# Optimization experiments

Hardware: AMD Instinct MI355X
Metric: run time of the kernel (lower is better)

The kernel has to match this reference:

```python
import jax, jax.numpy as jnp
from jax import lax
import numpy as np

B = 32        # graphs per batch
NN = 513      # nodes per graph (odd M so Y/Z head lengths match)
IN = 128      # input_dim
OUT = 256     # output_dim
T = 4         # edge_types
STEPS = 4     # ggnn propagation steps
DEG = 16
N = B * NN
E = N * DEG
CAT = IN + OUT


def setup_inputs() -> dict:
    key = jax.random.key(0)
    ks = jax.random.split(key, 16)
    f32 = jnp.float32
    feature = jax.random.normal(ks[0], (N, IN), f32)
    offs = (jnp.arange(B) * NN)[:, None]
    edge_src = (jax.random.randint(ks[1], (B, NN * DEG), 0, NN) + offs).reshape(-1)
    edge_dst = (jax.random.randint(ks[2], (B, NN * DEG), 0, NN) + offs).reshape(-1)
    edge_type = jax.random.randint(ks[3], (E,), 0, T)
    s = 1.0 / np.sqrt(OUT)
    W_msg = jax.random.normal(ks[4], (T, OUT, OUT), f32) * s      # [T, out, in] (torch Linear layout)
    b_msg = jnp.zeros((T, OUT), f32)
    gru_w_ih = jax.random.normal(ks[5], (3 * OUT, OUT), f32) * s
    gru_w_hh = jax.random.normal(ks[6], (3 * OUT, OUT), f32) * s
    gru_b_ih = jnp.zeros((3 * OUT,), f32)
    gru_b_hh = jnp.zeros((3 * OUT,), f32)
    conv1_w = jax.random.normal(ks[7], (OUT, OUT, 3), f32) * (1.0 / np.sqrt(OUT * 3))
    conv1_b = jnp.zeros((OUT,), f32)
    conv2_w = jax.random.normal(ks[8], (OUT, OUT, 1), f32) * s
    conv2_b = jnp.zeros((OUT,), f32)
    convc1_w = jax.random.normal(ks[9], (CAT, CAT, 3), f32) * (1.0 / np.sqrt(CAT * 3))
    convc1_b = jnp.zeros((CAT,), f32)
    convc2_w = jax.random.normal(ks[10], (CAT, CAT, 2), f32) * (1.0 / np.sqrt(CAT * 2))
    convc2_b = jnp.zeros((CAT,), f32)
    mlpy_w = jax.random.normal(ks[11], (1, OUT), f32) * s
    mlpy_b = jnp.zeros((1,), f32)
    mlpz_w = jax.random.normal(ks[12], (1, CAT), f32) * (1.0 / np.sqrt(CAT))
    mlpz_b = jnp.zeros((1,), f32)
    return dict(feature=feature, W_msg=W_msg, b_msg=b_msg,
                gru_w_ih=gru_w_ih, gru_w_hh=gru_w_hh, gru_b_ih=gru_b_ih, gru_b_hh=gru_b_hh,
                conv1_w=conv1_w, conv1_b=conv1_b, conv2_w=conv2_w, conv2_b=conv2_b,
                convc1_w=convc1_w, convc1_b=convc1_b, convc2_w=convc2_w, convc2_b=convc2_b,
                mlpy_w=mlpy_w, mlpy_b=mlpy_b, mlpz_w=mlpz_w, mlpz_b=mlpz_b,
                edge_src=edge_src, edge_dst=edge_dst, edge_type=edge_type)


def _conv1d(x, w, b):
    # x: [B, C_in, L], w: [C_out, C_in, K]
    y = lax.conv_general_dilated(x, w, (1,), 'VALID', dimension_numbers=('NCH', 'OIH', 'NCH'))
    return y + b[None, :, None]


def _maxpool1d(x, k, s):
    init = jnp.array(-jnp.inf, dtype=x.dtype)
    return lax.reduce_window(x, init, lax.max, (1, 1, k), (1, 1, s), 'VALID')


def _forward(feature, W_msg, b_msg, gru_w_ih, gru_w_hh, gru_b_ih, gru_b_hh,
             conv1_w, conv1_b, conv2_w, conv2_b, convc1_w, convc1_b, convc2_w, convc2_b,
             mlpy_w, mlpy_b, mlpz_w, mlpz_b, edge_src, edge_dst, edge_type):
    # --- GatedGraphConv (DGL semantics): zero-pad features to out_feats ---
    h = jnp.pad(feature, ((0, 0), (0, OUT - IN)))  # [N, OUT]
    for _ in range(STEPS):
        # per-etype linear on all nodes: hw[t] = h @ W_msg[t].T + b_msg[t]
        hw = jnp.einsum('nd,tod->tno', h, W_msg) + b_msg[:, None, :]   # [T, N, OUT]
        msg = hw[edge_type, edge_src]                                   # [E, OUT] gather
        a = jax.ops.segment_sum(msg, edge_dst, num_segments=N)          # [N, OUT] scatter-add
        # GRUCell(a, h) in torch gate order (r, z, n)
        gi = a @ gru_w_ih.T + gru_b_ih
        gh = h @ gru_w_hh.T + gru_b_hh
        ir, iz, inn = jnp.split(gi, 3, axis=-1)
        hr, hz, hn = jnp.split(gh, 3, axis=-1)
        r = jax.nn.sigmoid(ir + hr)
        z = jax.nn.sigmoid(iz + hz)
        n = jnp.tanh(inn + r * hn)
        h = (1.0 - z) * n + z * h
    outputs = h                                             # [N, OUT]
    ci = jnp.concatenate([outputs, feature], axis=-1)       # [N, OUT+IN]
    # batchify to [B, C, L]
    hi = outputs.reshape(B, NN, OUT).transpose(0, 2, 1)
    cb = ci.reshape(B, NN, CAT).transpose(0, 2, 1)
    Y1 = _maxpool1d(jax.nn.relu(_conv1d(hi, conv1_w, conv1_b)), 3, 2)
    Y2 = _maxpool1d(jax.nn.relu(_conv1d(Y1, conv2_w, conv2_b)), 2, 2).transpose(0, 2, 1)   # [B, 127, OUT]
    Z1 = _maxpool1d(jax.nn.relu(_conv1d(cb, convc1_w, convc1_b)), 3, 2)
    Z2 = _maxpool1d(jax.nn.relu(_conv1d(Z1, convc2_w, convc2_b)), 2, 2).transpose(0, 2, 1)  # [B, 127, CAT]
    before_avg = (Y2 @ mlpy_w.T + mlpy_b) * (Z2 @ mlpz_w.T + mlpz_b)   # [B, 127, 1]
    avg = before_avg.mean(axis=1)                                       # [B, 1]
    return jax.nn.sigmoid(avg).squeeze(-1)                              # [B]


def reference(feature, W_msg, b_msg, gru_w_ih, gru_w_hh, gru_b_ih, gru_b_hh,
              conv1_w, conv1_b, conv2_w, conv2_b, convc1_w, convc1_b, convc2_w, convc2_b,
              mlpy_w, mlpy_b, mlpz_w, mlpz_b, edge_src, edge_dst, edge_type):
    return _forward(feature, W_msg, b_msg, gru_w_ih, gru_w_hh, gru_b_ih, gru_b_hh,
                    conv1_w, conv1_b, conv2_w, conv2_b, convc1_w, convc1_b, convc2_w, convc2_b,
                    mlpy_w, mlpy_b, mlpz_w, mlpz_b, edge_src, edge_dst, edge_type)
```

## Files before the change

### kernel.cpp

```cpp
#include <hip/hip_runtime.h>

#define Bg    32
#define NNg   513
#define INF   128
#define OUTF  256
#define TT    4
#define NSTEP 4
#define DEGg  16
#define Ntot  (Bg*NNg)
#define Etot  (Ntot*DEGg)
#define CATF  (OUTF+INF)
#define SK    1056
#define NSB   65

typedef _Float16 h8_t __attribute__((ext_vector_type(8)));
typedef float    f4_t __attribute__((ext_vector_type(4)));

__global__ void pad_h_k(const float* __restrict__ feat, float* __restrict__ h,
                        _Float16* __restrict__ h16) {
  int idx = blockIdx.x*256 + threadIdx.x;
  if (idx >= Ntot*OUTF) return;
  int n = idx >> 8, c = idx & 255;
  float v = (c < INF) ? feat[n*INF + c] : 0.f;
  h[idx] = v;
  h16[idx] = (_Float16)v;
}

__global__ void cvt_k(const float* __restrict__ s, _Float16* __restrict__ d, int n) {
  int i = (blockIdx.x*256 + threadIdx.x) * 4;
  if (i >= n) return;
  float4 v = *reinterpret_cast<const float4*>(s + i);
  _Float16 o[4] = {(_Float16)v.x, (_Float16)v.y, (_Float16)v.z, (_Float16)v.w};
  *reinterpret_cast<ushort4*>(d + i) = *reinterpret_cast<ushort4*>(o);
}

__global__ void build_cb16_k(const _Float16* __restrict__ h16,
                             const float* __restrict__ feat,
                             _Float16* __restrict__ cb) {
  int idx = blockIdx.x*256 + threadIdx.x;
  if (idx >= Ntot*CATF) return;
  int n = idx / CATF, c = idx % CATF;
  cb[idx] = (c < OUTF) ? h16[n*OUTF + c] : (_Float16)feat[n*INF + (c - OUTF)];
}

__global__ void zero_int_k(int* __restrict__ p, int n) {
  int i = blockIdx.x*256 + threadIdx.x;
  if (i < n) p[i] = 0;
}

__global__ void hist_k(const int* __restrict__ dst, int* __restrict__ cnt) {
  int e = blockIdx.x*256 + threadIdx.x;
  if (e < Etot) atomicAdd(&cnt[dst[e]], 1);
}

__global__ void scan1_k(const int* __restrict__ cnt, int* __restrict__ rowptr,
                        int* __restrict__ bsum) {
  __shared__ int buf[256];
  int t = threadIdx.x;
  int i = blockIdx.x*256 + t;
  int v = (i < Ntot) ? cnt[i] : 0;
  buf[t] = v;
  __syncthreads();
  #pragma unroll
  for (int off = 1; off < 256; off <<= 1) {
    int x = (t >= off) ? buf[t - off] : 0;
    __syncthreads();
    buf[t] += x;
    __syncthreads();
  }
  if (i < Ntot) rowptr[i] = buf[t] - v;
  if (t == 255) bsum[blockIdx.x] = buf[255];
}

__global__ void scan2_k(int* __restrict__ bsum) {
  __shared__ int buf[256];
  int t = threadIdx.x;
  int v = (t < NSB) ? bsum[t] : 0;
  buf[t] = v;
  __syncthreads();
  #pragma unroll
  for (int off = 1; off < 256; off <<= 1) {
    int x = (t >= off) ? buf[t - off] : 0;
    __syncthreads();
    buf[t] += x;
    __syncthreads();
  }
  if (t < NSB) bsum[t] = buf[t] - v;
}

__global__ void scan3_k(int* __restrict__ rowptr, const int* __restrict__ bsum) {
  int i = blockIdx.x*256 + threadIdx.x;
  if (i < Ntot) rowptr[i] += bsum[blockIdx.x];
  if (i == 0) rowptr[Ntot] = Etot;
}

__global__ void fill_k(const int* __restrict__ dst, const int* __restrict__ rowptr,
                       int* __restrict__ cursor, int* __restrict__ eidx) {
  int e = blockIdx.x*256 + threadIdx.x;
  if (e < Etot) {
    int d = dst[e];
    int pos = atomicAdd(&cursor[d], 1);
    eidx[rowptr[d] + pos] = e;
  }
}

__global__ void gather_k(const _Float16* __restrict__ h16, const int* __restrict__ rowptr,
                         const int* __restrict__ eidx, const int* __restrict__ esrc,
                         const int* __restrict__ etyp, _Float16* __restrict__ s16) {
  __shared__ int src_s[128];
  __shared__ int typ_s[128];
  int n = blockIdx.x;
  int c = threadIdx.x;
  int s0 = rowptr[n], e0 = rowptr[n+1];
  float a0 = 0.f, a1 = 0.f, a2 = 0.f, a3 = 0.f;
  int c0 = 0, c1 = 0, c2 = 0, c3 = 0;
  for (int base = s0; base < e0; base += 128) {
    int m = e0 - base; if (m > 128) m = 128;
    if (c < m) {
      int ee = eidx[base + c];
      src_s[c] = esrc[ee];
      typ_s[c] = etyp[ee];
    }
    __syncthreads();
    for (int i = 0; i < m; ++i) {
      int t = typ_s[i];
      float v = (float)h16[(size_t)src_s[i]*256 + c];
      a0 += (t == 0) ? v : 0.f;
      a1 += (t == 1) ? v : 0.f;
      a2 += (t == 2) ? v : 0.f;
      a3 += (t == 3) ? v : 0.f;
      c0 += (t == 0); c1 += (t == 1); c2 += (t == 2); c3 += (t == 3);
    }
    __syncthreads();
  }
  size_t b = (size_t)n * SK;
  s16[b + 0*256 + c] = (_Float16)a0;
  s16[b + 1*256 + c] = (_Float16)a1;
  s16[b + 2*256 + c] = (_Float16)a2;
  s16[b + 3*256 + c] = (_Float16)a3;
  if (c < 32) {
    float cv = (c == 0) ? (float)c0 : (c == 1) ? (float)c1 :
               (c == 2) ? (float)c2 : (c == 3) ? (float)c3 : 0.f;
    s16[b + 1024 + c] = (_Float16)cv;
  }
}

__global__ void repack_wext_k(const float* __restrict__ Wmsg, const float* __restrict__ bmsg,
                              _Float16* __restrict__ wext) {
  int idx = blockIdx.x*256 + threadIdx.x;
  if (idx >= 256*SK) return;
  int co = idx / SK, k = idx % SK;
  float v;
  if (k < 1024)      { int t = k >> 8, ci = k & 255; v = Wmsg[((size_t)t*256 + co)*256 + ci]; }
  else if (k < 1028) { v = bmsg[(k - 1024)*256 + co]; }
  else               { v = 0.f; }
  wext[idx] = (_Float16)v;
}

__global__ void gru_gate_k(const float* __restrict__ gi, const float* __restrict__ gh,
                           float* __restrict__ h, _Float16* __restrict__ h16) {
  int idx = blockIdx.x*256 + threadIdx.x;
  if (idx >= Ntot*OUTF) return;
  int n = idx >> 8, g = idx & 255;
  const float* gin = gi + (size_t)n*768;
  const float* ghn = gh + (size_t)n*768;
  float r  = 1.f / (1.f + expf(-(gin[g]       + ghn[g])));
  float z  = 1.f / (1.f + expf(-(gin[256 + g] + ghn[256 + g])));
  float nn = tanhf(gin[512 + g] + r * ghn[512 + g]);
  float hv = h[idx];
  float o = (1.f - z) * nn + z * hv;
  h[idx] = o;
  h16[idx] = (_Float16)o;
}

template<typename OT>
__global__ void maxpool_k(const float* __restrict__ in, OT* __restrict__ out,
                          int Lin, int Lp, int C, int kwin) {
  int idx = blockIdx.x*256 + threadIdx.x;
  int total = Bg*Lp*C;
  if (idx >= total) return;
  int c = idx % C; int r = idx / C; int p = r % Lp; int b = r / Lp;
  const float* base = in + ((size_t)(b*Lin + 2*p))*C + c;
  float v = base[0];
  for (int w = 1; w < kwin; ++w) v = fmaxf(v, base[(size_t)w*C]);
  out[idx] = (OT)v;
}

__global__ void repack16_k(const float* __restrict__ w, _Float16* __restrict__ wk,
                           int Cout, int Cin, int K) {
  int idx = blockIdx.x*256 + threadIdx.x;
  int total = Cout*Cin*K;
  if (idx >= total) return;
  int ci = idx % Cin; int r = idx / Cin; int k = r % K; int co = r / K;
  wk[idx] = (_Float16)w[(co*Cin + ci)*K + k];
}

__global__ void head_k(const float* __restrict__ Y2, const float* __restrict__ Z2,
                       const float* __restrict__ wy, const float* __restrict__ by,
                       const float* __restrict__ wz, const float* __restrict__ bz,
                       float* __restrict__ out) {
  int b = blockIdx.x;
  int tid = threadIdx.x;
  __shared__ float red[128];
  float sum = 0.f;
  for (int p = tid; p < 127; p += 128) {
    const float* yr = Y2 + ((size_t)(b*127 + p))*OUTF;
    const float* zr = Z2 + ((size_t)(b*127 + p))*CATF;
    float yv = by[0], zv = bz[0];
    for (int c = 0; c < OUTF; ++c) yv = fmaf(yr[c], wy[c], yv);
    for (int c = 0; c < CATF; ++c) zv = fmaf(zr[c], wz[c], zv);
    sum += yv * zv;
  }
  red[tid] = sum;
  __syncthreads();
  for (int off = 64; off > 0; off >>= 1) {
    if (tid < off) red[tid] += red[tid + off];
    __syncthreads();
  }
  if (tid == 0) out[b] = 1.f / (1.f + expf(-red[0] / 127.f));
}

template<typename CT, bool RELU, bool MAPPED>
__global__ __launch_bounds__(256, 2) void hgemm(
    const _Float16* __restrict__ A, const _Float16* __restrict__ W,
    const float* __restrict__ bias, CT* __restrict__ C,
    int M, int Nout, int K, int arstride, int Lout, int NNodes) {
  __shared__ _Float16 As[128][40];
  __shared__ _Float16 Ws[128][40];
  int tid = threadIdx.x;
  int lane = tid & 63, wid = tid >> 6;
  int wm = wid >> 1, wn = wid & 1;
  int l15 = lane & 15, l4 = lane >> 4;
  int m0 = blockIdx.x * 128, n0 = blockIdx.y * 128;

  int s_row = tid >> 1;
  int s_col = (tid & 1) * 16;
  int m_s = m0 + s_row;
  bool a_ok = (m_s < M);
  int mc = a_ok ? m_s : (M - 1);
  int node = MAPPED ? (mc / Lout) * NNodes + (mc % Lout) : mc;
  const _Float16* a_src = A + (size_t)node * arstride + s_col;
  const _Float16* w_src = W + (size_t)(n0 + s_row) * K + s_col;

  f4_t acc[4][4] = {};

  for (int k0 = 0; k0 < K; k0 += 32) {
    if (k0) __syncthreads();
    int4 va0 = {0,0,0,0}, va1 = {0,0,0,0};
    if (a_ok) {
      const int4* ga = reinterpret_cast<const int4*>(a_src + k0);
      va0 = ga[0]; va1 = ga[1];
    }
    const int4* gw = reinterpret_cast<const int4*>(w_src + k0);
    int4 vw0 = gw[0], vw1 = gw[1];
    *reinterpret_cast<int4*>(&As[s_row][s_col])     = va0;
    *reinterpret_cast<int4*>(&As[s_row][s_col + 8]) = va1;
    *reinterpret_cast<int4*>(&Ws[s_row][s_col])     = vw0;
    *reinterpret_cast<int4*>(&Ws[s_row][s_col + 8]) = vw1;
    __syncthreads();

    h8_t af[4], bf[4];
    #pragma unroll
    for (int fm = 0; fm < 4; ++fm)
      af[fm] = *reinterpret_cast<const h8_t*>(&As[wm*64 + fm*16 + l15][l4*8]);
    #pragma unroll
    for (int fn = 0; fn < 4; ++fn)
      bf[fn] = *reinterpret_cast<const h8_t*>(&Ws[wn*64 + fn*16 + l15][l4*8]);
    #pragma unroll
    for (int fm = 0; fm < 4; ++fm)
      #pragma unroll
      for (int fn = 0; fn < 4; ++fn)
        acc[fm][fn] = __builtin_amdgcn_mfma_f32_16x16x32_f16(af[fm], bf[fn], acc[fm][fn], 0, 0, 0);
  }

  #pragma unroll
  for (int fn = 0; fn < 4; ++fn) {
    int col = n0 + wn*64 + fn*16 + l15;
    float bv = bias[col];
    #pragma unroll
    for (int fm = 0; fm < 4; ++fm) {
      #pragma unroll
      for (int i = 0; i < 4; ++i) {
        int m = m0 + wm*64 + fm*16 + l4*4 + i;
        if (m >= M) continue;
        float v = acc[fm][fn][i] + bv;
        if (RELU) v = fmaxf(v, 0.f);
        C[(size_t)m * Nout + col] = (CT)v;
      }
    }
  }
}

static inline int cdiv(int x, int y) { return (x + y - 1) / y; }

extern "C" void kernel_launch(void* const* d_in, const int* in_sizes, int n_in,
                              void* d_out, int out_size, void* d_ws, size_t ws_size,
                              hipStream_t stream) {
  const float* feature  = (const float*)d_in[0];
  const float* W_msg    = (const float*)d_in[1];
  const float* b_msg    = (const float*)d_in[2];
  const float* w_ih     = (const float*)d_in[3];
  const float* w_hh     = (const float*)d_in[4];
  const float* b_ih     = (const float*)d_in[5];
  const float* b_hh     = (const float*)d_in[6];
  const float* conv1_w  = (const float*)d_in[7];
  const float* conv1_b  = (const float*)d_in[8];
  const float* conv2_w  = (const float*)d_in[9];
  const float* conv2_b  = (const float*)d_in[10];
  const float* convc1_w = (const float*)d_in[11];
  const float* convc1_b = (const float*)d_in[12];
  const float* convc2_w = (const float*)d_in[13];
  const float* convc2_b = (const float*)d_in[14];
  const float* mlpy_w   = (const float*)d_in[15];
  const float* mlpy_b   = (const float*)d_in[16];
  const float* mlpz_w   = (const float*)d_in[17];
  const float* mlpz_b   = (const float*)d_in[18];
  const int*   esrc     = (const int*)d_in[19];
  const int*   edst     = (const int*)d_in[20];
  const int*   etyp     = (const int*)d_in[21];
  float* out = (float*)d_out;

  char* base = (char*)d_ws;
  size_t off = 0;
  auto alloc = [&](size_t bytes) { void* p = base + off; off = (off + bytes + 255) & ~(size_t)255; return p; };
  float*    h      = (float*)   alloc((size_t)Ntot*OUTF*4);
  _Float16* h16    = (_Float16*)alloc((size_t)Ntot*OUTF*2);
  _Float16* Wext16 = (_Float16*)alloc((size_t)256*SK*2);
  _Float16* wih16  = (_Float16*)alloc((size_t)768*256*2);
  _Float16* whh16  = (_Float16*)alloc((size_t)768*256*2);
  float*    bias0  = (float*)   alloc(256*4);
  int* rowptr = (int*)alloc((Ntot+1)*4);
  int* cnt    = (int*)alloc(Ntot*4);
  int* bsum   = (int*)alloc(NSB*4);
  int* eidx   = (int*)alloc((size_t)Etot*4);
  char* big   = (char*)alloc((size_t)Ntot*1536*4);
  float*    gi  = (float*)big;
  float*    gh  = gi + (size_t)Ntot*768;
  _Float16* s16 = (_Float16*)(big + (size_t)Ntot*768*4);
  _Float16* a16 = s16 + (size_t)Ntot*SK;
  float*    Y2   = (float*)big;
  float*    Z2   = Y2 + (size_t)Bg*127*OUTF;
  float*    y1   = Z2 + (size_t)Bg*127*CATF;
  float*    y2   = y1 + (size_t)Bg*511*OUTF;
  _Float16* p1   = (_Float16*)(y2 + (size_t)Bg*255*OUTF);
  _Float16* cb16 = p1 + (size_t)Bg*255*OUTF;
  float*    z1   = (float*)(cb16 + (size_t)Ntot*CATF);
  float*    z2   = z1 + (size_t)Bg*511*CATF;
  _Float16* pz1  = (_Float16*)(z2 + (size_t)Bg*254*CATF);
  _Float16* wk1  = pz1 + (size_t)Bg*255*CATF;
  _Float16* wkc1 = wk1 + (size_t)256*768;
  _Float16* wkc2 = wkc1 + (size_t)384*1152;
  _Float16* c2w16= wkc2 + (size_t)384*768;

  dim3 blk(256);

  pad_h_k<<<cdiv(Ntot*OUTF,256), blk, 0, stream>>>(feature, h, h16);
  repack_wext_k<<<cdiv(256*SK,256), blk, 0, stream>>>(W_msg, b_msg, Wext16);
  cvt_k<<<cdiv(768*256/4,256), blk, 0, stream>>>(w_ih, wih16, 768*256);
  cvt_k<<<cdiv(768*256/4,256), blk, 0, stream>>>(w_hh, whh16, 768*256);
  hipMemsetAsync(bias0, 0, 256*4, stream);

  zero_int_k<<<cdiv(Ntot,256), blk, 0, stream>>>(cnt, Ntot);
  hist_k<<<cdiv(Etot,256), blk, 0, stream>>>(edst, cnt);
  scan1_k<<<NSB, blk, 0, stream>>>(cnt, rowptr, bsum);
  scan2_k<<<1, blk, 0, stream>>>(bsum);
  scan3_k<<<NSB, blk, 0, stream>>>(rowptr, bsum);
  zero_int_k<<<cdiv(Ntot,256), blk, 0, stream>>>(cnt, Ntot);
  fill_k<<<cdiv(Etot,256), blk, 0, stream>>>(edst, rowptr, cnt, eidx);

  for (int s = 0; s < NSTEP; ++s) {
    gather_k<<<Ntot, blk, 0, stream>>>(h16, rowptr, eidx, esrc, etyp, s16);
    hgemm<_Float16,false,false><<<dim3(cdiv(Ntot,128), 2), blk, 0, stream>>>(
        s16, Wext16, bias0, a16, Ntot, 256, SK, SK, 0, 0);
    hgemm<float,false,false><<<dim3(cdiv(Ntot,128), 6), blk, 0, stream>>>(
        a16, wih16, b_ih, gi, Ntot, 768, 256, 256, 0, 0);
    hgemm<float,false,false><<<dim3(cdiv(Ntot,128), 6), blk, 0, stream>>>(
        h16, whh16, b_hh, gh, Ntot, 768, 256, 256, 0, 0);
    gru_gate_k<<<cdiv(Ntot*OUTF,256), blk, 0, stream>>>(gi, gh, h, h16);
  }

  repack16_k<<<cdiv(256*256*3,256), blk, 0, stream>>>(conv1_w,  wk1,  256, 256, 3);
  repack16_k<<<cdiv(384*384*3,256), blk, 0, stream>>>(convc1_w, wkc1, 384, 384, 3);
  repack16_k<<<cdiv(384*384*2,256), blk, 0, stream>>>(convc2_w, wkc2, 384, 384, 2);
  cvt_k<<<cdiv(256*256/4,256), blk, 0, stream>>>(conv2_w, c2w16, 256*256);

  hgemm<float,true,true><<<dim3(cdiv(Bg*511,128), 2), blk, 0, stream>>>(
      h16, wk1, conv1_b, y1, Bg*511, 256, 768, 256, 511, NNg);
  maxpool_k<_Float16><<<cdiv(Bg*255*256,256), blk, 0, stream>>>(y1, p1, 511, 255, 256, 3);
  hgemm<float,true,false><<<dim3(cdiv(Bg*255,128), 2), blk, 0, stream>>>(
      p1, c2w16, conv2_b, y2, Bg*255, 256, 256, 256, 0, 0);
  maxpool_k<float><<<cdiv(Bg*127*256,256), blk, 0, stream>>>(y2, Y2, 255, 127, 256, 2);

  build_cb16_k<<<cdiv(Ntot*CATF,256), blk, 0, stream>>>(h16, feature, cb16);
  hgemm<float,true,true><<<dim3(cdiv(Bg*511,128), 3), blk, 0, stream>>>(
      cb16, wkc1, convc1_b, z1, Bg*511, 384, 1152, 384, 511, NNg);
  maxpool_k<_Float16><<<cdiv(Bg*255*384,256), blk, 0, stream>>>(z1, pz1, 511, 255, 384, 3);
  hgemm<float,true,true><<<dim3(cdiv(Bg*254,128), 3), blk, 0, stream>>>(
      pz1, wkc2, convc2_b, z2, Bg*254, 384, 768, 384, 254, 255);
  maxpool_k<float><<<cdiv(Bg*127*384,256), blk, 0, stream>>>(z2, Z2, 254, 127, 384, 2);

  head_k<<<Bg, 128, 0, stream>>>(Y2, Z2, mlpy_w, mlpy_b, mlpz_w, mlpz_b, out);
}
```

Before: 896.8 us.

## Bucket edges by (dst,type) CSR and store GRU/conv intermediates in fp16

Builds the CSR keyed on destination node and edge type, and stores source ids directly, so the gather no longer does an indirect eidx lookup or per-edge type selects, and the per-type counts come from row pointers. The GRU gate GEMM outputs (gi, gh) and the first conv outputs (y1, z1) are now written in fp16, which halves that intermediate traffic. The gate kernel is vectorised to handle four channels per thread. The cost is extra rounding of pre-activation gate values and conv outputs to fp16.

```diff
diff --git a/kernel.cpp b/kernel.cpp
--- a/kernel.cpp
+++ b/kernel.cpp
@@ -11,9 +11,11 @@
 #define Etot  (Ntot*DEGg)
 #define CATF  (OUTF+INF)
 #define SK    1056
-#define NSB   65
+#define NB    (Ntot*TT)
+#define NSB2  129
 
 typedef _Float16 h8_t __attribute__((ext_vector_type(8)));
+typedef _Float16 h4_t __attribute__((ext_vector_type(4)));
 typedef float    f4_t __attribute__((ext_vector_type(4)));
 
 __global__ void pad_h_k(const float* __restrict__ feat, float* __restrict__ h,
@@ -48,17 +50,35 @@
   if (i < n) p[i] = 0;
 }
 
-__global__ void hist_k(const int* __restrict__ dst, int* __restrict__ cnt) {
+__global__ void hist_k(const int* __restrict__ dst, const int* __restrict__ typ,
+                       int* __restrict__ cnt) {
   int e = blockIdx.x*256 + threadIdx.x;
-  if (e < Etot) atomicAdd(&cnt[dst[e]], 1);
-}
-
-__global__ void scan1_k(const int* __restrict__ cnt, int* __restrict__ rowptr,
+  if (e < Etot) atomicAdd(&cnt[dst[e]*TT + typ[e]], 1);
+}
+
+__global__ void scan1_k(const int* __restrict__ cnt, int* __restrict__ rp2,
                         int* __restrict__ bsum) {
+  __shared__ int buf[512];
+  int t = threadIdx.x;
+  int i = blockIdx.x*512 + t;
+  int v = (i < NB) ? cnt[i] : 0;
+  buf[t] = v;
+  __syncthreads();
+  #pragma unroll
+  for (int off = 1; off < 512; off <<= 1) {
+    int x = (t >= off) ? buf[t - off] : 0;
+    __syncthreads();
+    buf[t] += x;
+    __syncthreads();
+  }
+  if (i < NB) rp2[i] = buf[t] - v;
+  if (t == 511) bsum[blockIdx.x] = buf[511];
+}
+
+__global__ void scan2_k(int* __restrict__ bsum) {
   __shared__ int buf[256];
   int t = threadIdx.x;
-  int i = blockIdx.x*256 + t;
-  int v = (i < Ntot) ? cnt[i] : 0;
+  int v = (t < NSB2) ? bsum[t] : 0;
   buf[t] = v;
   __syncthreads();
   #pragma unroll
@@ -68,69 +88,45 @@
     buf[t] += x;
     __syncthreads();
   }
-  if (i < Ntot) rowptr[i] = buf[t] - v;
-  if (t == 255) bsum[blockIdx.x] = buf[255];
-}
-
-__global__ void scan2_k(int* __restrict__ bsum) {
-  __shared__ int buf[256];
-  int t = threadIdx.x;
-  int v = (t < NSB) ? bsum[t] : 0;
-  buf[t] = v;
-  __syncthreads();
-  #pragma unroll
-  for (int off = 1; off < 256; off <<= 1) {
-    int x = (t >= off) ? buf[t - off] : 0;
-    __syncthreads();
-    buf[t] += x;
-    __syncthreads();
-  }
-  if (t < NSB) bsum[t] = buf[t] - v;
-}
-
-__global__ void scan3_k(int* __restrict__ rowptr, const int* __restrict__ bsum) {
-  int i = blockIdx.x*256 + threadIdx.x;
-  if (i < Ntot) rowptr[i] += bsum[blockIdx.x];
-  if (i == 0) rowptr[Ntot] = Etot;
-}
-
-__global__ void fill_k(const int* __restrict__ dst, const int* __restrict__ rowptr,
-                       int* __restrict__ cursor, int* __restrict__ eidx) {
+  if (t < NSB2) bsum[t] = buf[t] - v;
+}
+
+__global__ void scan3_k(int* __restrict__ rp2, const int* __restrict__ bsum) {
+  int i = blockIdx.x*512 + threadIdx.x;
+  if (i < NB) rp2[i] += bsum[blockIdx.x];
+  if (i == 0) rp2[NB] = Etot;
+}
+
+__global__ void fill_k(const int* __restrict__ dst, const int* __restrict__ typ,
+                       const int* __restrict__ src, const int* __restrict__ rp2,
+                       int* __restrict__ cursor, int* __restrict__ srcv) {
   int e = blockIdx.x*256 + threadIdx.x;
   if (e < Etot) {
-    int d = dst[e];
-    int pos = atomicAdd(&cursor[d], 1);
-    eidx[rowptr[d] + pos] = e;
-  }
-}
-
-__global__ void gather_k(const _Float16* __restrict__ h16, const int* __restrict__ rowptr,
-                         const int* __restrict__ eidx, const int* __restrict__ esrc,
-                         const int* __restrict__ etyp, _Float16* __restrict__ s16) {
+    int b = dst[e]*TT + typ[e];
+    int pos = atomicAdd(&cursor[b], 1);
+    srcv[rp2[b] + pos] = src[e];
+  }
+}
+
+__global__ void gather_k(const _Float16* __restrict__ h16, const int* __restrict__ rp2,
+                         const int* __restrict__ srcv, _Float16* __restrict__ s16) {
   __shared__ int src_s[128];
-  __shared__ int typ_s[128];
   int n = blockIdx.x;
   int c = threadIdx.x;
-  int s0 = rowptr[n], e0 = rowptr[n+1];
+  int b0 = rp2[TT*n], e1 = rp2[TT*n+1], e2 = rp2[TT*n+2], e3 = rp2[TT*n+3], e4 = rp2[TT*n+4];
   float a0 = 0.f, a1 = 0.f, a2 = 0.f, a3 = 0.f;
-  int c0 = 0, c1 = 0, c2 = 0, c3 = 0;
-  for (int base = s0; base < e0; base += 128) {
-    int m = e0 - base; if (m > 128) m = 128;
-    if (c < m) {
-      int ee = eidx[base + c];
-      src_s[c] = esrc[ee];
-      typ_s[c] = etyp[ee];
-    }
-    __syncthreads();
-    for (int i = 0; i < m; ++i) {
-      int t = typ_s[i];
-      float v = (float)h16[(size_t)src_s[i]*256 + c];
-      a0 += (t == 0) ? v : 0.f;
-      a1 += (t == 1) ? v : 0.f;
-      a2 += (t == 2) ? v : 0.f;
-      a3 += (t == 3) ? v : 0.f;
-      c0 += (t == 0); c1 += (t == 1); c2 += (t == 2); c3 += (t == 3);
-    }
+  for (int base = b0; base < e4; base += 128) {
+    int m = e4 - base; if (m > 128) m = 128;
+    if (c < m) src_s[c] = srcv[base + c];
+    __syncthreads();
+    int l1 = min(max(e1 - base, 0), m);
+    int l2 = min(max(e2 - base, 0), m);
+    int l3 = min(max(e3 - base, 0), m);
+    int i = 0;
+    for (; i < l1; ++i) a0 += (float)h16[(size_t)src_s[i]*256 + c];
+    for (; i < l2; ++i) a1 += (float)h16[(size_t)src_s[i]*256 + c];
+    for (; i < l3; ++i) a2 += (float)h16[(size_t)src_s[i]*256 + c];
+    for (; i < m;  ++i) a3 += (float)h16[(size_t)src_s[i]*256 + c];
     __syncthreads();
   }
   size_t b = (size_t)n * SK;
@@ -139,9 +135,8 @@
   s16[b + 2*256 + c] = (_Float16)a2;
   s16[b + 3*256 + c] = (_Float16)a3;
   if (c < 32) {
-    float cv = (c == 0) ? (float)c0 : (c == 1) ? (float)c1 :
-               (c == 2) ? (float)c2 : (c == 3) ? (float)c3 : 0.f;
-    s16[b + 1024 + c] = (_Float16)cv;
+    int cv = (c == 0) ? (e1-b0) : (c == 1) ? (e2-e1) : (c == 2) ? (e3-e2) : (c == 3) ? (e4-e3) : 0;
+    s16[b + 1024 + c] = (_Float16)(float)cv;
   }
 }
 
@@ -157,32 +152,48 @@
   wext[idx] = (_Float16)v;
 }
 
-__global__ void gru_gate_k(const float* __restrict__ gi, const float* __restrict__ gh,
+__global__ void gru_gate_k(const _Float16* __restrict__ gi, const _Float16* __restrict__ gh,
                            float* __restrict__ h, _Float16* __restrict__ h16) {
   int idx = blockIdx.x*256 + threadIdx.x;
-  if (idx >= Ntot*OUTF) return;
-  int n = idx >> 8, g = idx & 255;
-  const float* gin = gi + (size_t)n*768;
-  const float* ghn = gh + (size_t)n*768;
-  float r  = 1.f / (1.f + expf(-(gin[g]       + ghn[g])));
-  float z  = 1.f / (1.f + expf(-(gin[256 + g] + ghn[256 + g])));
-  float nn = tanhf(gin[512 + g] + r * ghn[512 + g]);
-  float hv = h[idx];
-  float o = (1.f - z) * nn + z * hv;
-  h[idx] = o;
-  h16[idx] = (_Float16)o;
-}
-
-template<typename OT>
-__global__ void maxpool_k(const float* __restrict__ in, OT* __restrict__ out,
+  if (idx >= Ntot*64) return;
+  int n = idx >> 6, g4 = (idx & 63) * 4;
+  const _Float16* gin = gi + (size_t)n*768 + g4;
+  const _Float16* ghn = gh + (size_t)n*768 + g4;
+  h4_t ir = *reinterpret_cast<const h4_t*>(gin);
+  h4_t iz = *reinterpret_cast<const h4_t*>(gin + 256);
+  h4_t in_ = *reinterpret_cast<const h4_t*>(gin + 512);
+  h4_t hr = *reinterpret_cast<const h4_t*>(ghn);
+  h4_t hz = *reinterpret_cast<const h4_t*>(ghn + 256);
+  h4_t hn = *reinterpret_cast<const h4_t*>(ghn + 512);
+  size_t hb = (size_t)n*256 + g4;
+  float4 hv = *reinterpret_cast<const float4*>(h + hb);
+  float hvv[4] = {hv.x, hv.y, hv.z, hv.w};
+  float ov[4];
+  _Float16 ov16[4];
+  #pragma unroll
+  for (int j = 0; j < 4; ++j) {
+    float r  = 1.f / (1.f + expf(-((float)ir[j] + (float)hr[j])));
+    float z  = 1.f / (1.f + expf(-((float)iz[j] + (float)hz[j])));
+    float nn = tanhf((float)in_[j] + r * (float)hn[j]);
+    float o = (1.f - z) * nn + z * hvv[j];
+    ov[j] = o;
+    ov16[j] = (_Float16)o;
+  }
+  float4 os = {ov[0], ov[1], ov[2], ov[3]};
+  *reinterpret_cast<float4*>(h + hb) = os;
+  *reinterpret_cast<ushort4*>(h16 + hb) = *reinterpret_cast<ushort4*>(ov16);
+}
+
+template<typename IT, typename OT>
+__global__ void maxpool_k(const IT* __restrict__ in, OT* __restrict__ out,
                           int Lin, int Lp, int C, int kwin) {
   int idx = blockIdx.x*256 + threadIdx.x;
   int total = Bg*Lp*C;
   if (idx >= total) return;
   int c = idx % C; int r = idx / C; int p = r % Lp; int b = r / Lp;
-  const float* base = in + ((size_t)(b*Lin + 2*p))*C + c;
-  float v = base[0];
-  for (int w = 1; w < kwin; ++w) v = fmaxf(v, base[(size_t)w*C]);
+  const IT* base = in + ((size_t)(b*Lin + 2*p))*C + c;
+  float v = (float)base[0];
+  for (int w = 1; w < kwin; ++w) v = fmaxf(v, (float)base[(size_t)w*C]);
   out[idx] = (OT)v;
 }
 
@@ -329,23 +340,23 @@
   _Float16* wih16  = (_Float16*)alloc((size_t)768*256*2);
   _Float16* whh16  = (_Float16*)alloc((size_t)768*256*2);
   float*    bias0  = (float*)   alloc(256*4);
-  int* rowptr = (int*)alloc((Ntot+1)*4);
-  int* cnt    = (int*)alloc(Ntot*4);
-  int* bsum   = (int*)alloc(NSB*4);
-  int* eidx   = (int*)alloc((size_t)Etot*4);
+  int* rp2    = (int*)alloc((NB+1)*4);
+  int* cnt    = (int*)alloc(NB*4);
+  int* bsum   = (int*)alloc(NSB2*4);
+  int* srcv   = (int*)alloc((size_t)Etot*4);
   char* big   = (char*)alloc((size_t)Ntot*1536*4);
-  float*    gi  = (float*)big;
-  float*    gh  = gi + (size_t)Ntot*768;
+  _Float16* gi  = (_Float16*)big;
+  _Float16* gh  = gi + (size_t)Ntot*768;
   _Float16* s16 = (_Float16*)(big + (size_t)Ntot*768*4);
   _Float16* a16 = s16 + (size_t)Ntot*SK;
   float*    Y2   = (float*)big;
   float*    Z2   = Y2 + (size_t)Bg*127*OUTF;
-  float*    y1   = Z2 + (size_t)Bg*127*CATF;
-  float*    y2   = y1 + (size_t)Bg*511*OUTF;
+  _Float16* y1   = (_Float16*)(Z2 + (size_t)Bg*127*CATF);
+  float*    y2   = (float*)(y1 + (size_t)Bg*511*OUTF);
   _Float16* p1   = (_Float16*)(y2 + (size_t)Bg*255*OUTF);
   _Float16* cb16 = p1 + (size_t)Bg*255*OUTF;
-  float*    z1   = (float*)(cb16 + (size_t)Ntot*CATF);
-  float*    z2   = z1 + (size_t)Bg*511*CATF;
+  _Float16* z1   = cb16 + (size_t)Ntot*CATF;
+  float*    z2   = (float*)(z1 + (size_t)Bg*511*CATF);
   _Float16* pz1  = (_Float16*)(z2 + (size_t)Bg*254*CATF);
   _Float16* wk1  = pz1 + (size_t)Bg*255*CATF;
   _Float16* wkc1 = wk1 + (size_t)256*768;
@@ -360,23 +371,23 @@
   cvt_k<<<cdiv(768*256/4,256), blk, 0, stream>>>(w_hh, whh16, 768*256);
   hipMemsetAsync(bias0, 0, 256*4, stream);
 
-  zero_int_k<<<cdiv(Ntot,256), blk, 0, stream>>>(cnt, Ntot);
-  hist_k<<<cdiv(Etot,256), blk, 0, stream>>>(edst, cnt);
-  scan1_k<<<NSB, blk, 0, stream>>>(cnt, rowptr, bsum);
+  zero_int_k<<<cdiv(NB,256), blk, 0, stream>>>(cnt, NB);
+  hist_k<<<cdiv(Etot,256), blk, 0, stream>>>(edst, etyp, cnt);
+  scan1_k<<<NSB2, 512, 0, stream>>>(cnt, rp2, bsum);
   scan2_k<<<1, blk, 0, stream>>>(bsum);
-  scan3_k<<<NSB, blk, 0, stream>>>(rowptr, bsum);
-  zero_int_k<<<cdiv(Ntot,256), blk, 0, stream>>>(cnt, Ntot);
-  fill_k<<<cdiv(Etot,256), blk, 0, stream>>>(edst, rowptr, cnt, eidx);
+  scan3_k<<<NSB2, 512, 0, stream>>>(rp2, bsum);
+  zero_int_k<<<cdiv(NB,256), blk, 0, stream>>>(cnt, NB);
+  fill_k<<<cdiv(Etot,256), blk, 0, stream>>>(edst, etyp, esrc, rp2, cnt, srcv);
 
   for (int s = 0; s < NSTEP; ++s) {
-    gather_k<<<Ntot, blk, 0, stream>>>(h16, rowptr, eidx, esrc, etyp, s16);
+    gather_k<<<Ntot, blk, 0, stream>>>(h16, rp2, srcv, s16);
     hgemm<_Float16,false,false><<<dim3(cdiv(Ntot,128), 2), blk, 0, stream>>>(
         s16, Wext16, bias0, a16, Ntot, 256, SK, SK, 0, 0);
-    hgemm<float,false,false><<<dim3(cdiv(Ntot,128), 6), blk, 0, stream>>>(
+    hgemm<_Float16,false,false><<<dim3(cdiv(Ntot,128), 6), blk, 0, stream>>>(
         a16, wih16, b_ih, gi, Ntot, 768, 256, 256, 0, 0);
-    hgemm<float,false,false><<<dim3(cdiv(Ntot,128), 6), blk, 0, stream>>>(
+    hgemm<_Float16,false,false><<<dim3(cdiv(Ntot,128), 6), blk, 0, stream>>>(
         h16, whh16, b_hh, gh, Ntot, 768, 256, 256, 0, 0);
-    gru_gate_k<<<cdiv(Ntot*OUTF,256), blk, 0, stream>>>(gi, gh, h, h16);
+    gru_gate_k<<<cdiv(Ntot*64,256), blk, 0, stream>>>(gi, gh, h, h16);
   }
 
   repack16_k<<<cdiv(256*256*3,256), blk, 0, stream>>>(conv1_w,  wk1,  256, 256, 3);
@@ -384,20 +395,20 @@
   repack16_k<<<cdiv(384*384*2,256), blk, 0, stream>>>(convc2_w, wkc2, 384, 384, 2);
   cvt_k<<<cdiv(256*256/4,256), blk, 0, stream>>>(conv2_w, c2w16, 256*256);
 
-  hgemm<float,true,true><<<dim3(cdiv(Bg*511,128), 2), blk, 0, stream>>>(
+  hgemm<_Float16,true,true><<<dim3(cdiv(Bg*511,128), 2), blk, 0, stream>>>(
       h16, wk1, conv1_b, y1, Bg*511, 256, 768, 256, 511, NNg);
-  maxpool_k<_Float16><<<cdiv(Bg*255*256,256), blk, 0, stream>>>(y1, p1, 511, 255, 256, 3);
+  maxpool_k<_Float16,_Float16><<<cdiv(Bg*255*256,256), blk, 0, stream>>>(y1, p1, 511, 255, 256, 3);
   hgemm<float,true,false><<<dim3(cdiv(Bg*255,128), 2), blk, 0, stream>>>(
       p1, c2w16, conv2_b, y2, Bg*255, 256, 256, 256, 0, 0);
-  maxpool_k<float><<<cdiv(Bg*127*256,256), blk, 0, stream>>>(y2, Y2, 255, 127, 256, 2);
+  maxpool_k<float,float><<<cdiv(Bg*127*256,256), blk, 0, stream>>>(y2, Y2, 255, 127, 256, 2);
 
   build_cb16_k<<<cdiv(Ntot*CATF,256), blk, 0, stream>>>(h16, feature, cb16);
-  hgemm<float,true,true><<<dim3(cdiv(Bg*511,128), 3), blk, 0, stream>>>(
+  hgemm<_Float16,true,true><<<dim3(cdiv(Bg*511,128), 3), blk, 0, stream>>>(
       cb16, wkc1, convc1_b, z1, Bg*511, 384, 1152, 384, 511, NNg);
-  maxpool_k<_Float16><<<cdiv(Bg*255*384,256), blk, 0, stream>>>(z1, pz1, 511, 255, 384, 3);
+  maxpool_k<_Float16,_Float16><<<cdiv(Bg*255*384,256), blk, 0, stream>>>(z1, pz1, 511, 255, 384, 3);
   hgemm<float,true,true><<<dim3(cdiv(Bg*254,128), 3), blk, 0, stream>>>(
       pz1, wkc2, convc2_b, z2, Bg*254, 384, 768, 384, 254, 255);
-  maxpool_k<float><<<cdiv(Bg*127*384,256), blk, 0, stream>>>(z2, Z2, 254, 127, 384, 2);
+  maxpool_k<float,float><<<cdiv(Bg*127*384,256), blk, 0, stream>>>(z2, Z2, 254, 127, 384, 2);
 
   head_k<<<Bg, 128, 0, stream>>>(Y2, Z2, mlpy_w, mlpy_b, mlpz_w, mlpz_b, out);
 }
```

After: 940.3 us. 1.05x slower.
